# Kernel optimization log

Measured on AMD Instinct MI355X. Metric: run time of the kernel, lower is better.

The kernel has to match this reference:

```python
import jax, jax.numpy as jnp
import numpy as np

DIM = 384
K = 7          # kernel_size
FINAL = 16     # final_size
DROP_P = 0.2


def setup_inputs() -> dict:
    key = jax.random.key(0)
    k1, k2, k3, k4, k5, k6 = jax.random.split(key, 6)
    hr_feats = jax.random.normal(k1, (8, DIM, 112, 112), jnp.float32)
    guidance = jnp.zeros((1,), jnp.float32)  # unused by forward
    dropout_u = jax.random.uniform(k2, (8, FINAL, FINAL, 1), jnp.float32)
    aw = jax.random.normal(k3, (DIM,), jnp.float32) / np.sqrt(DIM).astype(np.float32)
    ab = 0.01 * jax.random.normal(k4, (1,), jnp.float32)
    w = 1.0 + 0.01 * jax.random.normal(k5, (K, K), jnp.float32)
    b = 0.01 * jax.random.normal(k6, (K, K), jnp.float32)
    return {"hr_feats": hr_feats, "guidance": guidance, "dropout_u": dropout_u,
            "aw": aw, "ab": ab, "w": w, "b": b}


def _unfold_patches(x):
    # x: [b, c, h, w] -> [b, nH, nW, K*K, c], matching torch Unfold + reshape/permute
    bs, c, h, wd = x.shape
    stride = (h - K) // (FINAL - 1)
    nH = FINAL
    nW = FINAL * (wd // h)
    r = (jnp.arange(nH) * stride)[:, None] + jnp.arange(K)      # [nH, K]
    cc = (jnp.arange(nW) * stride)[:, None] + jnp.arange(K)     # [nW, K]
    # advanced indexing -> [b, c, nH, nW, K, K]
    patches = x[:, :, r[:, None, :, None], cc[None, :, None, :]]
    # (kh, kw) flattened row-major, channel last -> same ordering as torch Unfold
    return patches.transpose(0, 2, 3, 4, 5, 1).reshape(bs, nH, nW, K * K, c)


def reference(hr_feats, guidance, dropout_u, aw, ab, w, b):
    patches = _unfold_patches(hr_feats)                    # [b, H, W, P, C]
    # attention_net (eval-mode Dropout is identity): Linear(dim, 1)
    logits = jnp.einsum('bhwpc,c->bhwp', patches, aw) + ab[0]
    mask = (dropout_u > DROP_P).astype(logits.dtype)       # [b, H, W, 1]
    attn_logits = logits * mask * w.reshape(1, 1, 1, -1) + b.reshape(1, 1, 1, -1)
    attn = jax.nn.softmax(attn_logits, axis=-1)            # softmax over patches
    return jnp.einsum('bhwpc,bhwp->bchw', patches, attn)   # [b, C, H, W]
```

## Files before the change

kernel.cpp:

```cpp
#include <hip/hip_runtime.h>
#include <cmath>

#define DIM 384
#define IMG 112
#define IMG2 (IMG*IMG)
#define FINALN 16
#define PATCH 49
#define DROP_P 0.2f

__global__ __launch_bounds__(512) void kFused(const float* __restrict__ hr,
                                              const float* __restrict__ du,
                                              const float* __restrict__ aw,
                                              const float* __restrict__ ab,
                                              const float* __restrict__ wmat,
                                              const float* __restrict__ bmat,
                                              float* __restrict__ out) {
    __shared__ float sp[DIM * PATCH];
    __shared__ float s_aw[DIM];
    __shared__ float s_red[8 * PATCH];

    int tid = threadIdx.x;

    int id  = blockIdx.x;
    int nid = (id & 7) * 256 + (id >> 3);
    int b = nid >> 8;
    int h = (nid >> 4) & 15;
    int w = nid & 15;

    float duv = 0.f, abv = 0.f, wv = 0.f, bv = 0.f;
    if (tid < 64) {
        if (tid < PATCH) { wv = wmat[tid]; bv = bmat[tid]; }
        duv = du[(b << 8) + (h << 4) + w];
        abv = ab[0];
    }
    for (int i = tid; i < DIM; i += 512) s_aw[i] = aw[i];

    const float* base = hr + (size_t)b * DIM * IMG2 + (size_t)(7 * h) * IMG + 7 * w;
    #pragma unroll
    for (int k = 0; k < 6; ++k) {
        int r = tid + k * 512;
        if (r < DIM * 7) {
            int c = r / 7;
            int i = r - c * 7;
            const float* p = base + (size_t)c * IMG2 + i * IMG;
            float* d = sp + c * PATCH + i * 7;
            #pragma unroll
            for (int j = 0; j < 7; ++j) d[j] = p[j];
        }
    }
    __syncthreads();

    if (tid < 8 * PATCH) {
        int g = tid / PATCH;
        int p = tid - g * PATCH;
        int c0 = g * 48;
        float acc = 0.f;
        #pragma unroll 8
        for (int c = 0; c < 48; ++c)
            acc = fmaf(sp[(c0 + c) * PATCH + p], s_aw[c0 + c], acc);
        s_red[tid] = acc;
    }
    __syncthreads();

    if (tid < 64) {
        float al = -1e30f;
        if (tid < PATCH) {
            float logit = abv;
            #pragma unroll
            for (int g = 0; g < 8; ++g) logit += s_red[g * PATCH + tid];
            float mask = (duv > DROP_P) ? 1.0f : 0.0f;
            al = fmaf(logit * mask, wv, bv);
        }
        float m = al;
        #pragma unroll
        for (int d = 32; d >= 1; d >>= 1) m = fmaxf(m, __shfl_xor(m, d, 64));
        float e = (tid < PATCH) ? __expf(al - m) : 0.f;
        float s = e;
        #pragma unroll
        for (int d = 32; d >= 1; d >>= 1) s += __shfl_xor(s, d, 64);
        if (tid < PATCH) s_red[tid] = e / s;
    }
    __syncthreads();

    if (tid < DIM) {
        const float* pc = sp + tid * PATCH;
        float acc = 0.f;
        #pragma unroll
        for (int p = 0; p < PATCH; ++p)
            acc = fmaf(pc[p], s_red[p], acc);
        out[(((size_t)b * DIM + tid) * FINALN + h) * FINALN + w] = acc;
    }
}

extern "C" void kernel_launch(void* const* d_in, const int* in_sizes, int n_in,
                              void* d_out, int out_size, void* d_ws, size_t ws_size,
                              hipStream_t stream) {
    const float* hr   = (const float*)d_in[0];
    const float* du   = (const float*)d_in[2];
    const float* aw   = (const float*)d_in[3];
    const float* ab   = (const float*)d_in[4];
    const float* wmat = (const float*)d_in[5];
    const float* bmat = (const float*)d_in[6];
    float* out = (float*)d_out;

    kFused<<<2048, 512, 0, stream>>>(hr, du, aw, ab, wmat, bmat, out);
}
```

Before: 250.3 us.

## Process half-rows of patches per block with float4 coalesced loads

Restructures the kernel so each block handles eight adjacent patches in one output row. Logits are computed directly from global memory with float4 loads, then channels are streamed in 64-channel shared-memory slabs for the weighted sum. This replaces narrow scalar 7-wide loads with contiguous vector loads. In exchange it reads the input twice, launches far fewer blocks, and holds 49 attention weights per thread in registers.

```diff
diff --git a/kernel.cpp b/kernel.cpp
--- a/kernel.cpp
+++ b/kernel.cpp
@@ -8,87 +8,116 @@
 #define PATCH 49
 #define DROP_P 0.2f
 
-__global__ __launch_bounds__(512) void kFused(const float* __restrict__ hr,
-                                              const float* __restrict__ du,
-                                              const float* __restrict__ aw,
-                                              const float* __restrict__ ab,
-                                              const float* __restrict__ wmat,
-                                              const float* __restrict__ bmat,
-                                              float* __restrict__ out) {
-    __shared__ float sp[DIM * PATCH];
+#define SLABC 64
+#define SLABF (SLABC*392)
+
+__global__ __launch_bounds__(512) void kRow(const float* __restrict__ hr,
+                                            const float* __restrict__ du,
+                                            const float* __restrict__ aw,
+                                            const float* __restrict__ ab,
+                                            const float* __restrict__ wmat,
+                                            const float* __restrict__ bmat,
+                                            float* __restrict__ out) {
+    __shared__ float slab[SLABF];
     __shared__ float s_aw[DIM];
-    __shared__ float s_red[8 * PATCH];
+    __shared__ float attn_s[8 * 50];
 
-    int tid = threadIdx.x;
+    int tid  = threadIdx.x;
+    int id   = blockIdx.x;
+    int nid  = (id & 7) * 32 + (id >> 3);
+    int b  = nid >> 5;
+    int h  = (nid >> 1) & 15;
+    int wh = nid & 1;
 
-    int id  = blockIdx.x;
-    int nid = (id & 7) * 256 + (id >> 3);
-    int b = nid >> 8;
-    int h = (nid >> 4) & 15;
-    int w = nid & 15;
+    if (tid < DIM) s_aw[tid] = aw[tid];
 
-    float duv = 0.f, abv = 0.f, wv = 0.f, bv = 0.f;
-    if (tid < 64) {
-        if (tid < PATCH) { wv = wmat[tid]; bv = bmat[tid]; }
-        duv = du[(b << 8) + (h << 4) + w];
-        abv = ab[0];
-    }
-    for (int i = tid; i < DIM; i += 512) s_aw[i] = aw[i];
+    const float* base = hr + (size_t)b * DIM * IMG2 + (size_t)(7 * h) * IMG + 56 * wh;
 
-    const float* base = hr + (size_t)b * DIM * IMG2 + (size_t)(7 * h) * IMG + 7 * w;
-    #pragma unroll
-    for (int k = 0; k < 6; ++k) {
-        int r = tid + k * 512;
-        if (r < DIM * 7) {
-            int c = r / 7;
-            int i = r - c * 7;
-            const float* p = base + (size_t)c * IMG2 + i * IMG;
-            float* d = sp + c * PATCH + i * 7;
-            #pragma unroll
-            for (int j = 0; j < 7; ++j) d[j] = p[j];
+    int c_sub = tid / 98;
+    int q     = tid - c_sub * 98;
+    int i1 = q / 14, cq1 = q - i1 * 14;
+    __syncthreads();
+
+    if (tid < 392) {
+        const float* gp = base + (size_t)c_sub * IMG2 + i1 * IMG + 4 * cq1;
+        float l0 = 0.f, l1 = 0.f, l2 = 0.f, l3 = 0.f;
+        int awi = c_sub;
+        #pragma unroll 8
+        for (int it = 0; it < 96; ++it) {
+            float4 v = *reinterpret_cast<const float4*>(gp);
+            float av = s_aw[awi];
+            l0 = fmaf(v.x, av, l0);
+            l1 = fmaf(v.y, av, l1);
+            l2 = fmaf(v.z, av, l2);
+            l3 = fmaf(v.w, av, l3);
+            gp += (size_t)4 * IMG2;
+            awi += 4;
         }
+        float4 st = make_float4(l0, l1, l2, l3);
+        *reinterpret_cast<float4*>(&slab[c_sub * 400 + 4 * q]) = st;
     }
     __syncthreads();
 
-    if (tid < 8 * PATCH) {
-        int g = tid / PATCH;
-        int p = tid - g * PATCH;
-        int c0 = g * 48;
-        float acc = 0.f;
-        #pragma unroll 8
-        for (int c = 0; c < 48; ++c)
-            acc = fmaf(sp[(c0 + c) * PATCH + p], s_aw[c0 + c], acc);
-        s_red[tid] = acc;
-    }
-    __syncthreads();
-
-    if (tid < 64) {
+    {
+        int ww = tid >> 6, l = tid & 63;
         float al = -1e30f;
-        if (tid < PATCH) {
-            float logit = abv;
-            #pragma unroll
-            for (int g = 0; g < 8; ++g) logit += s_red[g * PATCH + tid];
+        if (l < PATCH) {
+            int li = l / 7, lj = l - li * 7;
+            int pos = li * 56 + 7 * ww + lj;
+            float logit = slab[pos] + slab[400 + pos] + slab[800 + pos] + slab[1200 + pos];
+            float duv  = du[(b << 8) + (h << 4) + (wh << 3) + ww];
             float mask = (duv > DROP_P) ? 1.0f : 0.0f;
-            al = fmaf(logit * mask, wv, bv);
+            al = fmaf((logit + ab[0]) * mask, wmat[l], bmat[l]);
         }
         float m = al;
         #pragma unroll
         for (int d = 32; d >= 1; d >>= 1) m = fmaxf(m, __shfl_xor(m, d, 64));
-        float e = (tid < PATCH) ? __expf(al - m) : 0.f;
+        float e = (l < PATCH) ? __expf(al - m) : 0.f;
         float s = e;
         #pragma unroll
         for (int d = 32; d >= 1; d >>= 1) s += __shfl_xor(s, d, 64);
-        if (tid < PATCH) s_red[tid] = e / s;
+        if (l < PATCH) attn_s[ww * 50 + l] = e / s;
     }
     __syncthreads();
 
-    if (tid < DIM) {
-        const float* pc = sp + tid * PATCH;
-        float acc = 0.f;
+    int wloc = tid & 7;
+    int cs   = tid >> 3;
+    float attw[PATCH];
+    #pragma unroll
+    for (int p = 0; p < PATCH; ++p) attw[p] = attn_s[wloc * 50 + p];
+
+    int goff[13], loff[13];
+    #pragma unroll
+    for (int k = 0; k < 13; ++k) {
+        int idx = tid + 512 * k;
+        int c = idx / 98, qq = idx - c * 98;
+        int ii = qq / 14, cq = qq - ii * 14;
+        goff[k] = c * IMG2 + ii * IMG + 4 * cq;
+        loff[k] = idx * 4;
+    }
+
+    size_t ob = ((size_t)b * DIM + cs) * 256 + (h << 4) + (wh << 3) + wloc;
+
+    for (int cc = 0; cc < 6; ++cc) {
+        const float* cb = base + (size_t)(cc * SLABC) * IMG2;
         #pragma unroll
-        for (int p = 0; p < PATCH; ++p)
-            acc = fmaf(pc[p], s_red[p], acc);
-        out[(((size_t)b * DIM + tid) * FINALN + h) * FINALN + w] = acc;
+        for (int k = 0; k < 12; ++k)
+            *reinterpret_cast<float4*>(&slab[loff[k]]) =
+                *reinterpret_cast<const float4*>(cb + goff[k]);
+        if (tid < 128)
+            *reinterpret_cast<float4*>(&slab[loff[12]]) =
+                *reinterpret_cast<const float4*>(cb + goff[12]);
+        __syncthreads();
+
+        float o = 0.f;
+        const float* sr = &slab[cs * 392 + 7 * wloc];
+        #pragma unroll
+        for (int p = 0; p < PATCH; ++p) {
+            const int pi = p / 7, pj = p - (p / 7) * 7;
+            o = fmaf(sr[pi * 56 + pj], attw[p], o);
+        }
+        out[ob + (size_t)(cc * SLABC) * 256] = o;
+        if (cc < 5) __syncthreads();
     }
 }
 
@@ -103,5 +132,5 @@
     const float* bmat = (const float*)d_in[6];
     float* out = (float*)d_out;
 
-    kFused<<<2048, 512, 0, stream>>>(hr, du, aw, ab, wmat, bmat, out);
+    kRow<<<256, 512, 0, stream>>>(hr, du, aw, ab, wmat, bmat, out);
 }
```

After: 242.1 us. -3.3%, faster.
